# Kernel optimization log

Measured on AMD Instinct MI355X. Metric: run time of the kernel, lower is better.

The kernel has to match this reference:

```python
import jax, jax.numpy as jnp
import numpy as np

TAIL_BOUND = 20.0  # B
NUM_BINS = 16      # K
G, I = 8, 64       # n_gaussians, n_inputs
BATCH = 16384


def _rqs_forward(x, W, H, D, B):
    """Monotonic rational-quadratic spline (Durkan et al.), forward direction.
    x: [Bt,G,I]; W,H: [G,I,K] logits; D: [G,I,K-1] raw derivatives.
    Matches torch module: widths/heights = 2*B*softmax(logits), derivs = softplus,
    boundary derivatives fixed to 1, identity outside [-B, B].
    """
    dt = x.dtype
    widths = 2.0 * B * jax.nn.softmax(W, axis=-1)          # [G,I,K], sums to 2B
    heights = 2.0 * B * jax.nn.softmax(H, axis=-1)
    g, i, K = widths.shape
    one = jnp.ones((g, i, 1), dt)
    derivs = jnp.concatenate([one, jax.nn.softplus(D), one], axis=-1)  # [G,I,K+1]
    negB = jnp.full((g, i, 1), -B, dt)
    cumw = jnp.concatenate([negB, -B + jnp.cumsum(widths, -1)], -1)    # [G,I,K+1] knot x
    cumh = jnp.concatenate([negB, -B + jnp.cumsum(heights, -1)], -1)   # [G,I,K+1] knot y
    delta = heights / widths                                            # bin slopes

    inside = (x >= -B) & (x <= B)
    xc = jnp.clip(x, -B, B)
    # bin search: index of bin containing xc (broadcast compare vs. K+1 knots)
    idx = jnp.clip(jnp.sum((xc[..., None] >= cumw[None]).astype(jnp.int32), axis=-1) - 1, 0, K - 1)  # [Bt,G,I]

    gi = jnp.arange(g)[:, None]
    ii = jnp.arange(i)[None, :]

    def gather(p, j):  # p: [G,I,*], j: [Bt,G,I] -> [Bt,G,I]
        return p[gi, ii, j]

    in_cw, in_w = gather(cumw, idx), gather(widths, idx)
    in_ch, in_h = gather(cumh, idx), gather(heights, idx)
    in_delta = gather(delta, idx)
    d0, d1 = gather(derivs, idx), gather(derivs, idx + 1)

    theta = (xc - in_cw) / in_w
    tt = theta * (1.0 - theta)
    denom = in_delta + (d0 + d1 - 2.0 * in_delta) * tt
    numer = in_h * (in_delta * theta * theta + d0 * tt)
    z_in = in_ch + numer / denom
    dnum = in_delta * in_delta * (d1 * theta * theta + 2.0 * in_delta * tt + d0 * (1.0 - theta) ** 2)
    ld_in = jnp.log(dnum) - 2.0 * jnp.log(denom)

    z = jnp.where(inside, z_in, x)
    ld = jnp.where(inside, ld_in, jnp.zeros((), dt))
    return z, ld


def setup_inputs() -> dict:
    key = jax.random.key(0)
    kx, kw, kh, kd = jax.random.split(key, 4)
    # scale x so points spread across many bins; a few land outside the tail bound
    x = jax.random.normal(kx, (BATCH, G, I), dtype=jnp.float32) * 12.0
    W = jax.random.normal(kw, (G, I, NUM_BINS), dtype=jnp.float32)
    H = jax.random.normal(kh, (G, I, NUM_BINS), dtype=jnp.float32)
    D = jax.random.normal(kd, (G, I, NUM_BINS - 1), dtype=jnp.float32)
    return {"x": x, "W": W, "H": H, "D": D}


def reference(x, W, H, D):
    return _rqs_forward(x, W, H, D, TAIL_BOUND)
```

## Files before the change

### kernel.cpp

```cpp
#include <hip/hip_runtime.h>
#include <math.h>

#define TAIL_B 20.0f
#define BATCH 16384
#define NELEM (BATCH * 512)
#define ROWS_PB 64
#define LDS_BYTES 104448

typedef float vf4 __attribute__((ext_vector_type(4)));

__global__ __launch_bounds__(1024, 4) void rqs_fused(
    const float* __restrict__ x, const float* __restrict__ W,
    const float* __restrict__ H, const float* __restrict__ D,
    float* __restrict__ out)
{
    extern __shared__ float s[];
    float* sCW = s;
    float* sCH = s + 8704;
    float* sDK = s + 17408;

    const int tid   = threadIdx.x;
    const int col   = tid & 511;
    const int rsub  = tid >> 9;
    const int rbase = blockIdx.x * ROWS_PB + rsub * 32;

    float xbA[8], xbB[8];
#pragma unroll
    for (int i = 0; i < 8; ++i)
        xbA[i] = x[(rbase + i) * 512 + col];

    {
        const int c    = tid >> 1;
        const int half = tid & 1;
        const float* Wg = W + c * 16 + half * 8;
        const float* Hg = H + c * 16 + half * 8;

        vf4 wa = *reinterpret_cast<const vf4*>(Wg);
        vf4 wb = *reinterpret_cast<const vf4*>(Wg + 4);
        vf4 ha = *reinterpret_cast<const vf4*>(Hg);
        vf4 hb = *reinterpret_cast<const vf4*>(Hg + 4);

        float mw = fmaxf(fmaxf(fmaxf(wa.x, wa.y), fmaxf(wa.z, wa.w)),
                         fmaxf(fmaxf(wb.x, wb.y), fmaxf(wb.z, wb.w)));
        float mh = fmaxf(fmaxf(fmaxf(ha.x, ha.y), fmaxf(ha.z, ha.w)),
                         fmaxf(fmaxf(hb.x, hb.y), fmaxf(hb.z, hb.w)));
        mw = fmaxf(mw, __shfl_xor(mw, 1));
        mh = fmaxf(mh, __shfl_xor(mh, 1));

        float ew[8] = {__expf(wa.x - mw), __expf(wa.y - mw), __expf(wa.z - mw), __expf(wa.w - mw),
                       __expf(wb.x - mw), __expf(wb.y - mw), __expf(wb.z - mw), __expf(wb.w - mw)};
        float eh[8] = {__expf(ha.x - mh), __expf(ha.y - mh), __expf(ha.z - mh), __expf(ha.w - mh),
                       __expf(hb.x - mh), __expf(hb.y - mh), __expf(hb.z - mh), __expf(hb.w - mh)};

        float sw = 0.0f, sh = 0.0f;
#pragma unroll
        for (int j = 0; j < 8; ++j) { sw += ew[j]; sh += eh[j]; }
        float swp = __shfl_xor(sw, 1), shp = __shfl_xor(sh, 1);
        float scw = (2.0f * TAIL_B) / (sw + swp);
        float sch = (2.0f * TAIL_B) / (sh + shp);

        float aw = half ? swp : 0.0f;
        float ah = half ? shp : 0.0f;

        const float* Dg = D + c * 15;
        float* cw = sCW + c * 17;
        float* ch = sCH + c * 17;
        float* dk = sDK + c * 17;
        if (!half) { cw[0] = -TAIL_B; ch[0] = -TAIL_B; dk[0] = 1.0f; }

#pragma unroll
        for (int j = 0; j < 8; ++j) {
            aw += ew[j]; ah += eh[j];
            int t = half * 8 + j + 1;
            cw[t] = -TAIL_B + aw * scw;
            ch[t] = -TAIL_B + ah * sch;
            float dv = 1.0f;
            if (t < 16) {
                float v = Dg[t - 1];
                dv = fmaxf(v, 0.0f) + __logf(1.0f + __expf(-fabsf(v)));
            }
            dk[t] = dv;
        }
    }
    __syncthreads();

    float kr[15];
#pragma unroll
    for (int t = 0; t < 15; ++t) kr[t] = sCW[col * 17 + 1 + t];

    auto compute8 = [&](const float (&xb)[8], int r0) {
#pragma unroll
        for (int i = 0; i < 8; ++i) {
            float xx = xb[i];
            bool  inside = (xx >= -TAIL_B) && (xx <= TAIL_B);
            float xc = fminf(fmaxf(xx, -TAIL_B), TAIL_B);

            int idx = 0;
#pragma unroll
            for (int t = 0; t < 15; ++t) idx += (xc >= kr[t]) ? 1 : 0;

            int p = col * 17 + idx;
            float k0  = sCW[p], k1  = sCW[p + 1];
            float ch0 = sCH[p], ch1 = sCH[p + 1];
            float d0  = sDK[p], d1  = sDK[p + 1];

            float invw  = __builtin_amdgcn_rcpf(k1 - k0);
            float hh    = ch1 - ch0;
            float de    = hh * invw;
            float theta = (xc - k0) * invw;
            float omt   = 1.0f - theta;
            float tt    = theta * omt;
            float denom = de + (d0 + d1 - 2.0f * de) * tt;
            float rden  = __builtin_amdgcn_rcpf(denom);
            float numer = hh * (de * theta * theta + d0 * tt);
            float zin   = ch0 + numer * rden;
            float dnum  = de * de * (d1 * theta * theta + 2.0f * de * tt + d0 * omt * omt);
            float ldin  = 0.6931471805599453f * __log2f(dnum * rden * rden);

            float z  = inside ? zin : xx;
            float ld = inside ? ldin : 0.0f;

            int addr = (r0 + i) * 512 + col;
            __builtin_nontemporal_store(z,  out + addr);
            __builtin_nontemporal_store(ld, out + NELEM + addr);
        }
    };

#pragma unroll
    for (int i = 0; i < 8; ++i) xbB[i] = x[(rbase + 8 + i) * 512 + col];
    compute8(xbA, rbase);

#pragma unroll
    for (int i = 0; i < 8; ++i) xbA[i] = x[(rbase + 16 + i) * 512 + col];
    compute8(xbB, rbase + 8);

#pragma unroll
    for (int i = 0; i < 8; ++i) xbB[i] = x[(rbase + 24 + i) * 512 + col];
    compute8(xbA, rbase + 16);

    compute8(xbB, rbase + 24);
}

extern "C" void kernel_launch(void* const* d_in, const int* in_sizes, int n_in,
                              void* d_out, int out_size, void* d_ws, size_t ws_size,
                              hipStream_t stream)
{
    const float* x = (const float*)d_in[0];
    const float* W = (const float*)d_in[1];
    const float* H = (const float*)d_in[2];
    const float* D = (const float*)d_in[3];
    float* out = (float*)d_out;

    hipFuncSetAttribute(reinterpret_cast<const void*>(&rqs_fused),
                        hipFuncAttributeMaxDynamicSharedMemorySize, LDS_BYTES);

    rqs_fused<<<BATCH / ROWS_PB, 1024, LDS_BYTES, stream>>>(x, W, H, D, out);
}
```

Baseline: 26.35 us.

## Compute width knots in registers, drop LDS knot table, halve rows per block

Each thread now computes the cumulative width knots for its column directly from W in registers, rather than building a shared-memory table and reading it back. The bin's left and right knots are picked with selects during the search, which removes two LDS loads per element. LDS usage drops by a third, launch bounds allow 8 waves per SIMD, and rows per block are halved so the grid doubles. The cost is a redundant softmax over W per thread, and the per-block H/D table setup is amortized over fewer rows.

```diff
diff --git a/kernel.cpp b/kernel.cpp
--- a/kernel.cpp
+++ b/kernel.cpp
@@ -4,75 +4,80 @@
 #define TAIL_B 20.0f
 #define BATCH 16384
 #define NELEM (BATCH * 512)
-#define ROWS_PB 64
-#define LDS_BYTES 104448
+#define ROWS_PB 32
+#define LDS_BYTES 69632
 
 typedef float vf4 __attribute__((ext_vector_type(4)));
 
-__global__ __launch_bounds__(1024, 4) void rqs_fused(
+__global__ __launch_bounds__(1024, 8) void rqs_fused(
     const float* __restrict__ x, const float* __restrict__ W,
     const float* __restrict__ H, const float* __restrict__ D,
     float* __restrict__ out)
 {
     extern __shared__ float s[];
-    float* sCW = s;
-    float* sCH = s + 8704;
-    float* sDK = s + 17408;
+    float* sCH = s;
+    float* sDK = s + 8704;
 
     const int tid   = threadIdx.x;
     const int col   = tid & 511;
     const int rsub  = tid >> 9;
-    const int rbase = blockIdx.x * ROWS_PB + rsub * 32;
+    const int rbase = blockIdx.x * ROWS_PB + rsub * 16;
 
-    float xbA[8], xbB[8];
+    float xA[4], xB[4];
 #pragma unroll
-    for (int i = 0; i < 8; ++i)
-        xbA[i] = x[(rbase + i) * 512 + col];
+    for (int i = 0; i < 4; ++i)
+        xA[i] = x[(rbase + i) * 512 + col];
+
+    float kr[15];
+    {
+        const float* Wg = W + col * 16;
+        vf4 a = *reinterpret_cast<const vf4*>(Wg);
+        vf4 b = *reinterpret_cast<const vf4*>(Wg + 4);
+        vf4 c = *reinterpret_cast<const vf4*>(Wg + 8);
+        vf4 d = *reinterpret_cast<const vf4*>(Wg + 12);
+        float e[16] = {a.x, a.y, a.z, a.w, b.x, b.y, b.z, b.w,
+                       c.x, c.y, c.z, c.w, d.x, d.y, d.z, d.w};
+        float mw = e[0];
+#pragma unroll
+        for (int k = 1; k < 16; ++k) mw = fmaxf(mw, e[k]);
+        float sum = 0.0f;
+#pragma unroll
+        for (int k = 0; k < 16; ++k) { e[k] = __expf(e[k] - mw); sum += e[k]; }
+        float scw = (2.0f * TAIL_B) * __builtin_amdgcn_rcpf(sum);
+        float run = 0.0f;
+#pragma unroll
+        for (int k = 0; k < 15; ++k) { run += e[k]; kr[k] = -TAIL_B + run * scw; }
+    }
 
     {
         const int c    = tid >> 1;
         const int half = tid & 1;
-        const float* Wg = W + c * 16 + half * 8;
         const float* Hg = H + c * 16 + half * 8;
-
-        vf4 wa = *reinterpret_cast<const vf4*>(Wg);
-        vf4 wb = *reinterpret_cast<const vf4*>(Wg + 4);
         vf4 ha = *reinterpret_cast<const vf4*>(Hg);
         vf4 hb = *reinterpret_cast<const vf4*>(Hg + 4);
 
-        float mw = fmaxf(fmaxf(fmaxf(wa.x, wa.y), fmaxf(wa.z, wa.w)),
-                         fmaxf(fmaxf(wb.x, wb.y), fmaxf(wb.z, wb.w)));
         float mh = fmaxf(fmaxf(fmaxf(ha.x, ha.y), fmaxf(ha.z, ha.w)),
                          fmaxf(fmaxf(hb.x, hb.y), fmaxf(hb.z, hb.w)));
-        mw = fmaxf(mw, __shfl_xor(mw, 1));
         mh = fmaxf(mh, __shfl_xor(mh, 1));
 
-        float ew[8] = {__expf(wa.x - mw), __expf(wa.y - mw), __expf(wa.z - mw), __expf(wa.w - mw),
-                       __expf(wb.x - mw), __expf(wb.y - mw), __expf(wb.z - mw), __expf(wb.w - mw)};
         float eh[8] = {__expf(ha.x - mh), __expf(ha.y - mh), __expf(ha.z - mh), __expf(ha.w - mh),
                        __expf(hb.x - mh), __expf(hb.y - mh), __expf(hb.z - mh), __expf(hb.w - mh)};
-
-        float sw = 0.0f, sh = 0.0f;
+        float sh = 0.0f;
 #pragma unroll
-        for (int j = 0; j < 8; ++j) { sw += ew[j]; sh += eh[j]; }
-        float swp = __shfl_xor(sw, 1), shp = __shfl_xor(sh, 1);
-        float scw = (2.0f * TAIL_B) / (sw + swp);
+        for (int j = 0; j < 8; ++j) sh += eh[j];
+        float shp = __shfl_xor(sh, 1);
         float sch = (2.0f * TAIL_B) / (sh + shp);
-
-        float aw = half ? swp : 0.0f;
-        float ah = half ? shp : 0.0f;
+        float ah  = half ? shp : 0.0f;
 
         const float* Dg = D + c * 15;
-        float* cw = sCW + c * 17;
         float* ch = sCH + c * 17;
         float* dk = sDK + c * 17;
-        if (!half) { cw[0] = -TAIL_B; ch[0] = -TAIL_B; dk[0] = 1.0f; }
+        if (!half) { ch[0] = -TAIL_B; dk[0] = 1.0f; }
 
 #pragma unroll
         for (int j = 0; j < 8; ++j) {
-            aw += ew[j]; ah += eh[j];
+            ah += eh[j];
             int t = half * 8 + j + 1;
-            cw[t] = -TAIL_B + aw * scw;
             ch[t] = -TAIL_B + ah * sch;
             float dv = 1.0f;
             if (t < 16) {
@@ -84,42 +89,48 @@
     }
     __syncthreads();
 
-    float kr[15];
+    auto eval1 = [&](float xx, float& z, float& ld) {
+        bool  inside = (xx >= -TAIL_B) && (xx <= TAIL_B);
+        float xc = fminf(fmaxf(xx, -TAIL_B), TAIL_B);
+
+        int   idx = 0;
+        float k0 = -TAIL_B, k1 = TAIL_B;
 #pragma unroll
-    for (int t = 0; t < 15; ++t) kr[t] = sCW[col * 17 + 1 + t];
+        for (int t = 0; t < 15; ++t) {
+            bool c = xc >= kr[t];
+            idx += c ? 1 : 0;
+            k0 = c ? kr[t] : k0;
+        }
+#pragma unroll
+        for (int t = 14; t >= 0; --t)
+            k1 = (xc < kr[t]) ? kr[t] : k1;
 
-    auto compute8 = [&](const float (&xb)[8], int r0) {
+        int p = col * 17 + idx;
+        float ch0 = sCH[p], ch1 = sCH[p + 1];
+        float d0  = sDK[p], d1  = sDK[p + 1];
+
+        float invw  = __builtin_amdgcn_rcpf(k1 - k0);
+        float hh    = ch1 - ch0;
+        float de    = hh * invw;
+        float theta = (xc - k0) * invw;
+        float omt   = 1.0f - theta;
+        float tt    = theta * omt;
+        float denom = de + (d0 + d1 - 2.0f * de) * tt;
+        float rden  = __builtin_amdgcn_rcpf(denom);
+        float numer = hh * (de * theta * theta + d0 * tt);
+        float zin   = ch0 + numer * rden;
+        float dnum  = de * de * (d1 * theta * theta + 2.0f * de * tt + d0 * omt * omt);
+        float ldin  = 0.6931471805599453f * __log2f(dnum * rden * rden);
+
+        z  = inside ? zin : xx;
+        ld = inside ? ldin : 0.0f;
+    };
+
+    auto compute4 = [&](const float (&xb)[4], int r0) {
 #pragma unroll
-        for (int i = 0; i < 8; ++i) {
-            float xx = xb[i];
-            bool  inside = (xx >= -TAIL_B) && (xx <= TAIL_B);
-            float xc = fminf(fmaxf(xx, -TAIL_B), TAIL_B);
-
-            int idx = 0;
-#pragma unroll
-            for (int t = 0; t < 15; ++t) idx += (xc >= kr[t]) ? 1 : 0;
-
-            int p = col * 17 + idx;
-            float k0  = sCW[p], k1  = sCW[p + 1];
-            float ch0 = sCH[p], ch1 = sCH[p + 1];
-            float d0  = sDK[p], d1  = sDK[p + 1];
-
-            float invw  = __builtin_amdgcn_rcpf(k1 - k0);
-            float hh    = ch1 - ch0;
-            float de    = hh * invw;
-            float theta = (xc - k0) * invw;
-            float omt   = 1.0f - theta;
-            float tt    = theta * omt;
-            float denom = de + (d0 + d1 - 2.0f * de) * tt;
-            float rden  = __builtin_amdgcn_rcpf(denom);
-            float numer = hh * (de * theta * theta + d0 * tt);
-            float zin   = ch0 + numer * rden;
-            float dnum  = de * de * (d1 * theta * theta + 2.0f * de * tt + d0 * omt * omt);
-            float ldin  = 0.6931471805599453f * __log2f(dnum * rden * rden);
-
-            float z  = inside ? zin : xx;
-            float ld = inside ? ldin : 0.0f;
-
+        for (int i = 0; i < 4; ++i) {
+            float z, ld;
+            eval1(xb[i], z, ld);
             int addr = (r0 + i) * 512 + col;
             __builtin_nontemporal_store(z,  out + addr);
             __builtin_nontemporal_store(ld, out + NELEM + addr);
@@ -127,18 +138,18 @@
     };
 
 #pragma unroll
-    for (int i = 0; i < 8; ++i) xbB[i] = x[(rbase + 8 + i) * 512 + col];
-    compute8(xbA, rbase);
+    for (int i = 0; i < 4; ++i) xB[i] = x[(rbase + 4 + i) * 512 + col];
+    compute4(xA, rbase);
 
 #pragma unroll
-    for (int i = 0; i < 8; ++i) xbA[i] = x[(rbase + 16 + i) * 512 + col];
-    compute8(xbB, rbase + 8);
+    for (int i = 0; i < 4; ++i) xA[i] = x[(rbase + 8 + i) * 512 + col];
+    compute4(xB, rbase + 4);
 
 #pragma unroll
-    for (int i = 0; i < 8; ++i) xbB[i] = x[(rbase + 24 + i) * 512 + col];
-    compute8(xbA, rbase + 16);
+    for (int i = 0; i < 4; ++i) xB[i] = x[(rbase + 12 + i) * 512 + col];
+    compute4(xA, rbase + 8);
 
-    compute8(xbB, rbase + 24);
+    compute4(xB, rbase + 12);
 }
 
 extern "C" void kernel_launch(void* const* d_in, const int* in_sizes, int n_in,
```

Result: slower. 35.55 us (+34.9%).
